# Optimization experiments

Measured on AMD Instinct MI355X. Metric: run time of the kernel, lower is better.

The kernel has to match this reference:

```python
import jax, jax.numpy as jnp
import numpy as np

SCORE_THR = 0.5
IOU_THR = 0.5
N_ANCHORS = 8400  # standard YOLO 640x640 anchor count


def setup_inputs() -> dict:
    key = jax.random.key(0)
    # [1, 5, N]: channels are (cx, cy, w, h, person_conf); uniform keeps boxes/scores in [0,1)
    yolo_raw_out = jax.random.uniform(key, (1, 5, N_ANCHORS), dtype=jnp.float32)
    return {"yolo_raw_out": yolo_raw_out}


def _pairwise_iou(b):
    # b: [N,4] xyxy
    area = (b[:, 2] - b[:, 0]) * (b[:, 3] - b[:, 1])          # [N]
    lt = jnp.maximum(b[:, None, :2], b[None, :, :2])          # [N,N,2]
    rb = jnp.minimum(b[:, None, 2:], b[None, :, 2:])          # [N,N,2]
    wh = jnp.clip(rb - lt, 0.0)
    inter = wh[..., 0] * wh[..., 1]                           # [N,N]
    union = area[:, None] + area[None, :] - inter
    return inter / jnp.maximum(union, 1e-9)


def reference(yolo_raw_out):
    # permute(0,2,1).squeeze(0) -> [N,5]
    raw = yolo_raw_out[0].T
    cx, cy, w, h = raw[:, 0], raw[:, 1], raw[:, 2], raw[:, 3]
    scores = raw[:, 4]
    # cxcywh -> xyxy (torchvision.ops.box_convert)
    xyxy = jnp.stack([cx - w / 2, cy - h / 2, cx + w / 2, cy + h / 2], axis=-1)

    valid = scores >= SCORE_THR
    # sort by score descending; invalid boxes pushed to the end
    order = jnp.argsort(-jnp.where(valid, scores, -jnp.inf))
    sb = xyxy[order]          # [N,4] sorted boxes
    ss = scores[order]        # [N]
    sv = valid[order]         # [N] score-threshold mask

    iou = _pairwise_iou(sb)   # [N,N]
    n = ss.shape[0]
    idx = jnp.arange(n)

    # Greedy NMS: in score order, an active (kept, valid) box suppresses all
    # lower-scored boxes with IoU > threshold. Faithful to torchvision.ops.nms.
    def step(keep, i):
        active = keep[i]
        suppress = (iou[i] > IOU_THR) & (idx > i) & active
        return keep & ~suppress, None

    keep, _ = jax.lax.scan(step, sv, idx)

    # Fixed-shape output: kept rows carry (x1,y1,x2,y2,score); suppressed/filtered rows zeroed.
    out = jnp.concatenate([sb, ss[:, None]], axis=1) * keep[:, None].astype(ss.dtype)
    return out
```

## Files before the change

### kernel.cpp

```cpp
#include <hip/hip_runtime.h>
#include <cstdint>

#define N_ANCH 8400
#define CBLK 132
#define SCORE_THR 0.5f
#define NDIAG 8

typedef unsigned long long u64;
typedef unsigned int u32;

__device__ __forceinline__ u64 sort_key(float s, int idx) {
  u32 k32 = (s >= SCORE_THR) ? ~__float_as_uint(s) : 0xFFFFFFFFu;
  return ((u64)k32 << 32) | (u32)idx;
}

__device__ __forceinline__ u64 rfl64(u64 v) {
  u32 lo = (u32)__builtin_amdgcn_readfirstlane((int)(u32)v);
  u32 hi = (u32)__builtin_amdgcn_readfirstlane((int)(u32)(v >> 32));
  return ((u64)hi << 32) | lo;
}

__global__ void __launch_bounds__(256) rank_kernel(const float* __restrict__ raw,
                                                   float4* __restrict__ sbox,
                                                   float* __restrict__ sscore) {
  #pragma clang fp contract(off)
  int tid = blockIdx.x * 256 + threadIdx.x;
  int wid = tid >> 6, lane = tid & 63;
  int base = wid * 4;
  float sl = raw[4 * N_ANCH + base + (lane & 3)];
  float s0 = __shfl(sl, 0), s1 = __shfl(sl, 1);
  float s2 = __shfl(sl, 2), s3 = __shfl(sl, 3);
  u64 k0 = sort_key(s0, base),     k1 = sort_key(s1, base + 1);
  u64 k2 = sort_key(s2, base + 2), k3 = sort_key(s3, base + 3);
  int c0 = 0, c1 = 0, c2 = 0, c3 = 0;
  #pragma unroll 2
  for (int j = lane; j < N_ANCH; j += 64) {
    float sj = raw[4 * N_ANCH + j];
    u64 kj = sort_key(sj, j);
    c0 += kj < k0; c1 += kj < k1; c2 += kj < k2; c3 += kj < k3;
  }
  #pragma unroll
  for (int d = 1; d < 64; d <<= 1) {
    c0 += __shfl_xor(c0, d, 64); c1 += __shfl_xor(c1, d, 64);
    c2 += __shfl_xor(c2, d, 64); c3 += __shfl_xor(c3, d, 64);
  }
  if (lane < 4) {
    int row = base + lane;
    int cnt = (lane == 0) ? c0 : (lane == 1) ? c1 : (lane == 2) ? c2 : c3;
    float sc = (lane == 0) ? s0 : (lane == 1) ? s1 : (lane == 2) ? s2 : s3;
    float cx = raw[row], cy = raw[N_ANCH + row];
    float w = raw[2 * N_ANCH + row], h = raw[3 * N_ANCH + row];
    float hw = w * 0.5f, hh = h * 0.5f;
    sbox[cnt] = make_float4(cx - hw, cy - hh, cx + hw, cy + hh);
    sscore[cnt] = sc;
  }
}

__global__ void __launch_bounds__(256) mask_kernel(const float4* __restrict__ sbox,
                                                   const float* __restrict__ sscore,
                                                   u64* __restrict__ mask,
                                                   u64* __restrict__ wlo_t) {
  #pragma clang fp contract(off)
  int cb = blockIdx.x;
  int i0 = blockIdx.y * 256;
  if (cb + 7 < (i0 >> 6)) return;
  if (!(sscore[i0] >= SCORE_THR)) return;
  if (!(sscore[cb * 64] >= SCORE_THR)) return;
  int t = threadIdx.x;
  __shared__ float4 cbox[64];
  __shared__ float carea[64];
  int j0 = cb * 64;
  if (t < 64) {
    int j = j0 + t;
    float4 bj = (j < N_ANCH) ? sbox[j] : make_float4(0.f, 0.f, 0.f, 0.f);
    cbox[t] = bj;
    carea[t] = (bj.z - bj.x) * (bj.w - bj.y);
  }
  __syncthreads();
  int i = i0 + t;
  if (i >= N_ANCH) return;
  float4 bi = sbox[i];
  float ai = (bi.z - bi.x) * (bi.w - bi.y);
  u64 wHi = 0, wLo = 0;
  for (int jj = 0; jj < 64; ++jj) {
    int jg = j0 + jj;
    float4 bb = cbox[jj];
    float ltx = fmaxf(bi.x, bb.x), lty = fmaxf(bi.y, bb.y);
    float rbx = fminf(bi.z, bb.z), rby = fminf(bi.w, bb.w);
    float wx = fmaxf(rbx - ltx, 0.f), wy = fmaxf(rby - lty, 0.f);
    float inter = wx * wy;
    float uni = (ai + carea[jj]) - inter;
    float iou = inter / fmaxf(uni, 1e-9f);
    bool sup = (iou > 0.5f) && (jg < N_ANCH);
    wHi |= (u64)(sup && (jg > i)) << jj;
    wLo |= (u64)(sup && (jg < i)) << jj;
  }
  int rb = i >> 6;
  int d = rb - cb;
  if (d < 0) {
    mask[(u64)i * CBLK + cb] = wHi;
  } else if (d < NDIAG) {
    wlo_t[((u64)d * CBLK + rb) * 64 + (i & 63)] = wLo;
  }
}

__global__ void __launch_bounds__(512, 1) nms_kernel(const float4* __restrict__ sbox,
                                                     const float* __restrict__ sscore,
                                                     const u64* __restrict__ mask,
                                                     const u64* __restrict__ wlo_t,
                                                     float* __restrict__ out) {
  __shared__ u64 keepw[CBLK + 4];
  __shared__ u64 rem[CBLK + 4];
  int tid = threadIdx.x;
  int wave = tid >> 6, lane = tid & 63;

  float s0 = sscore[lane * 132];
  u64 pb = __ballot(s0 >= SCORE_THR);
  int cnt1 = (int)__popcll(pb);
  int n_valid = 0;
  if (cnt1 > 0) {
    int a = (cnt1 - 1) * 132 + 1;
    int i1 = a + 3 * lane;
    float t1 = (i1 + 0 < N_ANCH) ? sscore[i1 + 0] : -1.f;
    float t2 = (i1 + 1 < N_ANCH) ? sscore[i1 + 1] : -1.f;
    float t3 = (i1 + 2 < N_ANCH) ? sscore[i1 + 2] : -1.f;
    u64 q1 = __ballot(t1 >= SCORE_THR);
    u64 q2 = __ballot(t2 >= SCORE_THR);
    u64 q3 = __ballot(t3 >= SCORE_THR);
    n_valid = a + (int)__popcll(q1) + (int)__popcll(q2) + (int)__popcll(q3);
  }
  int VB = (n_valid + 63) >> 6;
  int NG = (VB + 3) >> 2;

  for (int b = tid; b < CBLK + 4; b += 512) { keepw[b] = 0; rem[b] = 0; }

  int rs = (wave - 1) * 37;
  int nr = 256 - rs; if (nr > 37) nr = 37;

  u64 cur[26], nxt[26];
  auto wt = [&](int d, int b) -> u64 {
    return wlo_t[((u64)d * CBLK + b) * 64 + lane];
  };
  auto load_w0 = [&](int g, u64* R) {
    int b = 4 * g;
    bool k1 = (b + 1 < VB), k2 = (b + 2 < VB), k3 = (b + 3 < VB);
    R[0] = wt(0, b);
    R[1] = k1 ? wt(0, b + 1) : 0ull;
    R[2] = k2 ? wt(0, b + 2) : 0ull;
    R[3] = k3 ? wt(0, b + 3) : 0ull;
    R[4] = k1 ? wt(1, b + 1) : 0ull;
    R[5] = k2 ? wt(2, b + 2) : 0ull;
    R[6] = k2 ? wt(1, b + 2) : 0ull;
    R[7] = k3 ? wt(3, b + 3) : 0ull;
    R[8] = k3 ? wt(2, b + 3) : 0ull;
    R[9] = k3 ? wt(1, b + 3) : 0ull;
    #pragma unroll
    for (int m = 0; m < 4; ++m) {
      int c = b + 4 + m;
      bool ok = (c < VB);
      #pragma unroll
      for (int j = 0; j < 4; ++j)
        R[10 + m * 4 + j] = ok ? wt(4 + m - j, c) : 0ull;
    }
  };
  auto fixpoint = [&](u64 colw, u64 act) -> u64 {
    u64 U = act, K = 0;
    while (U) {
      u64 covered = __ballot((colw & U) != 0ull);
      u64 nk = U & ~covered;
      u64 supp = __ballot((colw & nk) != 0ull);
      K |= nk;
      U &= ~(nk | supp);
    }
    return K;
  };

  u64 P0 = 0, P1 = 0, P2 = 0, P3 = 0;

  if (wave == 0 && NG > 0) load_w0(0, cur);

  for (int g = 0; g < NG; ++g) {
    asm volatile("s_waitcnt lgkmcnt(0)\ns_barrier" ::: "memory");

    if (wave == 0) {
      __builtin_amdgcn_s_setprio(1);
      int b = 4 * g;
      u64 r0 = rem[b], r1 = rem[b + 1], r2 = rem[b + 2], r3 = rem[b + 3];
      if (g > 0) {
        #pragma unroll
        for (int i = 0; i < 26; ++i) cur[i] = nxt[i];
      }
      if (g + 1 < NG) load_w0(g + 1, nxt);

      int remn = n_valid - b * 64;
      u64 vm0, vm1, vm2, vm3;
      {
        int m0 = remn, m1 = remn - 64, m2 = remn - 128, m3 = remn - 192;
        vm0 = (m0 >= 64) ? ~0ull : ((m0 <= 0) ? 0ull : ((1ull << m0) - 1ull));
        vm1 = (m1 >= 64) ? ~0ull : ((m1 <= 0) ? 0ull : ((1ull << m1) - 1ull));
        vm2 = (m2 >= 64) ? ~0ull : ((m2 <= 0) ? 0ull : ((1ull << m2) - 1ull));
        vm3 = (m3 >= 64) ? ~0ull : ((m3 <= 0) ? 0ull : ((1ull << m3) - 1ull));
      }
      u64 act0 = vm0 & ~(rfl64(r0) | P0);
      u64 act1 = vm1 & ~(rfl64(r1) | P1);
      u64 act2 = vm2 & ~(rfl64(r2) | P2);
      u64 act3 = vm3 & ~(rfl64(r3) | P3);

      u64 kw0 = fixpoint(cur[0], act0);
      u64 s1 = __ballot((cur[4] & kw0) != 0ull);
      u64 kw1 = fixpoint(cur[1], act1 & ~s1);
      u64 s2 = __ballot(((cur[5] & kw0) | (cur[6] & kw1)) != 0ull);
      u64 kw2 = fixpoint(cur[2], act2 & ~s2);
      u64 s3 = __ballot(((cur[7] & kw0) | (cur[8] & kw1) | (cur[9] & kw2)) != 0ull);
      u64 kw3 = fixpoint(cur[3], act3 & ~s3);

      if (lane == 0) {
        keepw[b] = kw0; keepw[b + 1] = kw1;
        keepw[b + 2] = kw2; keepw[b + 3] = kw3;
      }

      P0 = __ballot(((cur[10] & kw0) | (cur[11] & kw1) |
                     (cur[12] & kw2) | (cur[13] & kw3)) != 0ull);
      P1 = __ballot(((cur[14] & kw0) | (cur[15] & kw1) |
                     (cur[16] & kw2) | (cur[17] & kw3)) != 0ull);
      P2 = __ballot(((cur[18] & kw0) | (cur[19] & kw1) |
                     (cur[20] & kw2) | (cur[21] & kw3)) != 0ull);
      P3 = __ballot(((cur[22] & kw0) | (cur[23] & kw1) |
                     (cur[24] & kw2) | (cur[25] & kw3)) != 0ull);
      __builtin_amdgcn_s_setprio(0);
    } else if (g >= 1) {
      int e = g - 1;
      int base = 4 * e + 8;
      if (base < VB) {
        int wi = rs >> 6, sh = rs & 63;
        u64 lo = keepw[4 * e + wi];
        u64 hi = (sh + nr > 64 && wi < 3) ? keepw[4 * e + wi + 1] : 0ull;
        u64 window = sh ? ((lo >> sh) | (hi << (64 - sh))) : lo;
        window = rfl64(window);
        const u64* pr = mask + (u64)(256 * e + rs) * CBLK;
        int cL = base + lane;
        bool okL = (cL < VB);
        u64 acc = 0;
        #pragma unroll
        for (int r = 0; r < 37; ++r) {
          bool bit = (r < nr) && (((window >> r) & 1ull) != 0ull);
          u64 v = (bit && okL) ? pr[(u64)r * CBLK + cL] : 0ull;
          acc |= v;
        }
        if (okL && acc) atomicOr((unsigned long long*)&rem[cL], acc);
        if (base + 64 < VB) {
          int cH = cL + 64;
          bool okH = (cH < VB);
          u64 acc2 = 0;
          #pragma unroll
          for (int r = 0; r < 37; ++r) {
            bool bit = (r < nr) && (((window >> r) & 1ull) != 0ull);
            u64 v = (bit && okH) ? pr[(u64)r * CBLK + cH] : 0ull;
            acc2 |= v;
          }
          if (okH && acc2) atomicOr((unsigned long long*)&rem[cH], acc2);
        }
      }
    }
  }
  __syncthreads();

  for (int r2 = tid; r2 < N_ANCH; r2 += 512) {
    u64 kv = keepw[r2 >> 6];
    bool kp = (kv >> (r2 & 63)) & 1ull;
    float4 b4 = sbox[r2];
    float sc = sscore[r2];
    float* o = out + r2 * 5;
    o[0] = kp ? b4.x : 0.f;
    o[1] = kp ? b4.y : 0.f;
    o[2] = kp ? b4.z : 0.f;
    o[3] = kp ? b4.w : 0.f;
    o[4] = kp ? sc : 0.f;
  }
}

extern "C" void kernel_launch(void* const* d_in, const int* in_sizes, int n_in,
                              void* d_out, int out_size, void* d_ws, size_t ws_size,
                              hipStream_t stream) {
  const float* raw = (const float*)d_in[0];
  float* out = (float*)d_out;
  char* ws = (char*)d_ws;
  float4* sbox = (float4*)ws;
  float* sscore = (float*)(ws + 8448 * 16);
  u64* mask = (u64*)(ws + 8448 * 16 + 8448 * 4);
  u64* wlo_t = (u64*)(ws + 8448 * 16 + 8448 * 4 + (size_t)N_ANCH * CBLK * 8);

  rank_kernel<<<525, 256, 0, stream>>>(raw, sbox, sscore);
  mask_kernel<<<dim3(CBLK, 33), 256, 0, stream>>>(sbox, sscore, mask, wlo_t);
  nms_kernel<<<1, 512, 0, stream>>>(sbox, sscore, mask, wlo_t, out);
}
```

Before: 131.6 us.

## Merge four per-word NMS fixpoints into one joint loop; vectorize rank score loads

The serial NMS resolver in wave 0 used to run four fixpoint loops one after another, each block word waiting on the previous one. It now iterates all four words together, so the ballots for different words can overlap and the serial chain of dependent iterations gets shorter. Each round may do more ballots, since it always evaluates all four words. Separately, the rank kernel reads scores as float4 and compares four candidates per lane per iteration, cutting load instructions and loop trips.

```diff
diff --git a/kernel.cpp b/kernel.cpp
--- a/kernel.cpp
+++ b/kernel.cpp
@@ -27,17 +27,22 @@
   int tid = blockIdx.x * 256 + threadIdx.x;
   int wid = tid >> 6, lane = tid & 63;
   int base = wid * 4;
-  float sl = raw[4 * N_ANCH + base + (lane & 3)];
-  float s0 = __shfl(sl, 0), s1 = __shfl(sl, 1);
-  float s2 = __shfl(sl, 2), s3 = __shfl(sl, 3);
-  u64 k0 = sort_key(s0, base),     k1 = sort_key(s1, base + 1);
-  u64 k2 = sort_key(s2, base + 2), k3 = sort_key(s3, base + 3);
+  const float* sc = raw + 4 * N_ANCH;
+  float4 sv = *(const float4*)(sc + base);
+  u64 k0 = sort_key(sv.x, base),     k1 = sort_key(sv.y, base + 1);
+  u64 k2 = sort_key(sv.z, base + 2), k3 = sort_key(sv.w, base + 3);
   int c0 = 0, c1 = 0, c2 = 0, c3 = 0;
-  #pragma unroll 2
-  for (int j = lane; j < N_ANCH; j += 64) {
-    float sj = raw[4 * N_ANCH + j];
-    u64 kj = sort_key(sj, j);
-    c0 += kj < k0; c1 += kj < k1; c2 += kj < k2; c3 += kj < k3;
+  for (int it = 0; it < 33; ++it) {
+    int j = it * 256 + (lane << 2);
+    if (j < N_ANCH) {
+      float4 q = *(const float4*)(sc + j);
+      u64 a0 = sort_key(q.x, j),     a1 = sort_key(q.y, j + 1);
+      u64 a2 = sort_key(q.z, j + 2), a3 = sort_key(q.w, j + 3);
+      c0 += (a0 < k0) + (a1 < k0) + (a2 < k0) + (a3 < k0);
+      c1 += (a0 < k1) + (a1 < k1) + (a2 < k1) + (a3 < k1);
+      c2 += (a0 < k2) + (a1 < k2) + (a2 < k2) + (a3 < k2);
+      c3 += (a0 < k3) + (a1 < k3) + (a2 < k3) + (a3 < k3);
+    }
   }
   #pragma unroll
   for (int d = 1; d < 64; d <<= 1) {
@@ -47,12 +52,12 @@
   if (lane < 4) {
     int row = base + lane;
     int cnt = (lane == 0) ? c0 : (lane == 1) ? c1 : (lane == 2) ? c2 : c3;
-    float sc = (lane == 0) ? s0 : (lane == 1) ? s1 : (lane == 2) ? s2 : s3;
+    float s = (lane == 0) ? sv.x : (lane == 1) ? sv.y : (lane == 2) ? sv.z : sv.w;
     float cx = raw[row], cy = raw[N_ANCH + row];
     float w = raw[2 * N_ANCH + row], h = raw[3 * N_ANCH + row];
     float hw = w * 0.5f, hh = h * 0.5f;
     sbox[cnt] = make_float4(cx - hw, cy - hh, cx + hw, cy + hh);
-    sscore[cnt] = sc;
+    sscore[cnt] = s;
   }
 }
 
@@ -163,17 +168,6 @@
         R[10 + m * 4 + j] = ok ? wt(4 + m - j, c) : 0ull;
     }
   };
-  auto fixpoint = [&](u64 colw, u64 act) -> u64 {
-    u64 U = act, K = 0;
-    while (U) {
-      u64 covered = __ballot((colw & U) != 0ull);
-      u64 nk = U & ~covered;
-      u64 supp = __ballot((colw & nk) != 0ull);
-      K |= nk;
-      U &= ~(nk | supp);
-    }
-    return K;
-  };
 
   u64 P0 = 0, P1 = 0, P2 = 0, P3 = 0;
 
@@ -201,18 +195,32 @@
         vm2 = (m2 >= 64) ? ~0ull : ((m2 <= 0) ? 0ull : ((1ull << m2) - 1ull));
         vm3 = (m3 >= 64) ? ~0ull : ((m3 <= 0) ? 0ull : ((1ull << m3) - 1ull));
       }
-      u64 act0 = vm0 & ~(rfl64(r0) | P0);
-      u64 act1 = vm1 & ~(rfl64(r1) | P1);
-      u64 act2 = vm2 & ~(rfl64(r2) | P2);
-      u64 act3 = vm3 & ~(rfl64(r3) | P3);
-
-      u64 kw0 = fixpoint(cur[0], act0);
-      u64 s1 = __ballot((cur[4] & kw0) != 0ull);
-      u64 kw1 = fixpoint(cur[1], act1 & ~s1);
-      u64 s2 = __ballot(((cur[5] & kw0) | (cur[6] & kw1)) != 0ull);
-      u64 kw2 = fixpoint(cur[2], act2 & ~s2);
-      u64 s3 = __ballot(((cur[7] & kw0) | (cur[8] & kw1) | (cur[9] & kw2)) != 0ull);
-      u64 kw3 = fixpoint(cur[3], act3 & ~s3);
+      u64 U0 = vm0 & ~(rfl64(r0) | P0);
+      u64 U1 = vm1 & ~(rfl64(r1) | P1);
+      u64 U2 = vm2 & ~(rfl64(r2) | P2);
+      u64 U3 = vm3 & ~(rfl64(r3) | P3);
+
+      u64 K0 = 0, K1 = 0, K2 = 0, K3 = 0;
+      while (U0 | U1 | U2 | U3) {
+        u64 p0 = cur[0] & U0;
+        u64 p1 = (cur[4] & U0) | (cur[1] & U1);
+        u64 p2 = (cur[5] & U0) | (cur[6] & U1) | (cur[2] & U2);
+        u64 p3 = (cur[7] & U0) | (cur[8] & U1) | (cur[9] & U2) | (cur[3] & U3);
+        u64 c0 = __ballot(p0 != 0ull);
+        u64 c1 = __ballot(p1 != 0ull);
+        u64 c2 = __ballot(p2 != 0ull);
+        u64 c3 = __ballot(p3 != 0ull);
+        u64 n0 = U0 & ~c0, n1 = U1 & ~c1, n2 = U2 & ~c2, n3 = U3 & ~c3;
+        u64 s0 = __ballot((cur[0] & n0) != 0ull);
+        u64 s1 = __ballot(((cur[4] & n0) | (cur[1] & n1)) != 0ull);
+        u64 s2 = __ballot(((cur[5] & n0) | (cur[6] & n1) | (cur[2] & n2)) != 0ull);
+        u64 s3 = __ballot(((cur[7] & n0) | (cur[8] & n1) | (cur[9] & n2) |
+                           (cur[3] & n3)) != 0ull);
+        K0 |= n0; K1 |= n1; K2 |= n2; K3 |= n3;
+        U0 &= ~(n0 | s0); U1 &= ~(n1 | s1);
+        U2 &= ~(n2 | s2); U3 &= ~(n3 | s3);
+      }
+      u64 kw0 = K0, kw1 = K1, kw2 = K2, kw3 = K3;
 
       if (lane == 0) {
         keepw[b] = kw0; keepw[b + 1] = kw1;
```

Result: no change. 133.8 us (+1.7%).

## Fuse rank, mask and NMS stages into one cooperative kernel with grid syncs

Applied to the files above, without the earlier changes.

Merges the three launches into a single cooperative kernel of 256 blocks that runs the ranking, mask building and serial NMS phases, separated by grid-wide syncs, with the NMS done by block 0. This removes two kernel launch gaps and the inter-kernel drain. The ranking loop also switches to float4 loads that compare four candidates per lane. In exchange, grid.sync carries its own cost, mask tiles are now 512 rows per task with a strided task loop, and the old three-kernel path is kept as a fallback if the cooperative launch fails.

```diff
diff --git a/kernel.cpp b/kernel.cpp
--- a/kernel.cpp
+++ b/kernel.cpp
@@ -1,10 +1,14 @@
 #include <hip/hip_runtime.h>
+#include <hip/hip_cooperative_groups.h>
 #include <cstdint>
 
 #define N_ANCH 8400
 #define CBLK 132
 #define SCORE_THR 0.5f
 #define NDIAG 8
+#define NBLK 256
+
+namespace cg = cooperative_groups;
 
 typedef unsigned long long u64;
 typedef unsigned int u32;
@@ -20,24 +24,29 @@
   return ((u64)hi << 32) | lo;
 }
 
-__global__ void __launch_bounds__(256) rank_kernel(const float* __restrict__ raw,
-                                                   float4* __restrict__ sbox,
-                                                   float* __restrict__ sscore) {
+
+__device__ __forceinline__ void rank_task(const float* __restrict__ raw,
+                                          float4* __restrict__ sbox,
+                                          float* __restrict__ sscore,
+                                          int t5, int lane) {
   #pragma clang fp contract(off)
-  int tid = blockIdx.x * 256 + threadIdx.x;
-  int wid = tid >> 6, lane = tid & 63;
-  int base = wid * 4;
-  float sl = raw[4 * N_ANCH + base + (lane & 3)];
-  float s0 = __shfl(sl, 0), s1 = __shfl(sl, 1);
-  float s2 = __shfl(sl, 2), s3 = __shfl(sl, 3);
-  u64 k0 = sort_key(s0, base),     k1 = sort_key(s1, base + 1);
-  u64 k2 = sort_key(s2, base + 2), k3 = sort_key(s3, base + 3);
+  const float* sc = raw + 4 * N_ANCH;
+  int base = t5 * 4;
+  float4 sv = *(const float4*)(sc + base);
+  u64 k0 = sort_key(sv.x, base),     k1 = sort_key(sv.y, base + 1);
+  u64 k2 = sort_key(sv.z, base + 2), k3 = sort_key(sv.w, base + 3);
   int c0 = 0, c1 = 0, c2 = 0, c3 = 0;
-  #pragma unroll 2
-  for (int j = lane; j < N_ANCH; j += 64) {
-    float sj = raw[4 * N_ANCH + j];
-    u64 kj = sort_key(sj, j);
-    c0 += kj < k0; c1 += kj < k1; c2 += kj < k2; c3 += kj < k3;
+  for (int it = 0; it < 33; ++it) {
+    int j = it * 256 + (lane << 2);
+    if (j < N_ANCH) {
+      float4 q = *(const float4*)(sc + j);
+      u64 a0 = sort_key(q.x, j),     a1 = sort_key(q.y, j + 1);
+      u64 a2 = sort_key(q.z, j + 2), a3 = sort_key(q.w, j + 3);
+      c0 += (a0 < k0) + (a1 < k0) + (a2 < k0) + (a3 < k0);
+      c1 += (a0 < k1) + (a1 < k1) + (a2 < k1) + (a3 < k1);
+      c2 += (a0 < k2) + (a1 < k2) + (a2 < k2) + (a3 < k2);
+      c3 += (a0 < k3) + (a1 < k3) + (a2 < k3) + (a3 < k3);
+    }
   }
   #pragma unroll
   for (int d = 1; d < 64; d <<= 1) {
@@ -47,38 +56,22 @@
   if (lane < 4) {
     int row = base + lane;
     int cnt = (lane == 0) ? c0 : (lane == 1) ? c1 : (lane == 2) ? c2 : c3;
-    float sc = (lane == 0) ? s0 : (lane == 1) ? s1 : (lane == 2) ? s2 : s3;
+    float s = (lane == 0) ? sv.x : (lane == 1) ? sv.y : (lane == 2) ? sv.z : sv.w;
     float cx = raw[row], cy = raw[N_ANCH + row];
     float w = raw[2 * N_ANCH + row], h = raw[3 * N_ANCH + row];
     float hw = w * 0.5f, hh = h * 0.5f;
     sbox[cnt] = make_float4(cx - hw, cy - hh, cx + hw, cy + hh);
-    sscore[cnt] = sc;
-  }
-}
-
-__global__ void __launch_bounds__(256) mask_kernel(const float4* __restrict__ sbox,
-                                                   const float* __restrict__ sscore,
-                                                   u64* __restrict__ mask,
-                                                   u64* __restrict__ wlo_t) {
+    sscore[cnt] = s;
+  }
+}
+
+__device__ __forceinline__ void mask_row(const float4* __restrict__ sbox,
+                                         u64* __restrict__ mask,
+                                         u64* __restrict__ wlo_t,
+                                         const float4* cbox, const float* carea,
+                                         int i, int cb) {
   #pragma clang fp contract(off)
-  int cb = blockIdx.x;
-  int i0 = blockIdx.y * 256;
-  if (cb + 7 < (i0 >> 6)) return;
-  if (!(sscore[i0] >= SCORE_THR)) return;
-  if (!(sscore[cb * 64] >= SCORE_THR)) return;
-  int t = threadIdx.x;
-  __shared__ float4 cbox[64];
-  __shared__ float carea[64];
   int j0 = cb * 64;
-  if (t < 64) {
-    int j = j0 + t;
-    float4 bj = (j < N_ANCH) ? sbox[j] : make_float4(0.f, 0.f, 0.f, 0.f);
-    cbox[t] = bj;
-    carea[t] = (bj.z - bj.x) * (bj.w - bj.y);
-  }
-  __syncthreads();
-  int i = i0 + t;
-  if (i >= N_ANCH) return;
   float4 bi = sbox[i];
   float ai = (bi.z - bi.x) * (bi.w - bi.y);
   u64 wHi = 0, wLo = 0;
@@ -104,16 +97,13 @@
   }
 }
 
-__global__ void __launch_bounds__(512, 1) nms_kernel(const float4* __restrict__ sbox,
-                                                     const float* __restrict__ sscore,
-                                                     const u64* __restrict__ mask,
-                                                     const u64* __restrict__ wlo_t,
-                                                     float* __restrict__ out) {
-  __shared__ u64 keepw[CBLK + 4];
-  __shared__ u64 rem[CBLK + 4];
-  int tid = threadIdx.x;
-  int wave = tid >> 6, lane = tid & 63;
-
+__device__ void nms_body(const float4* __restrict__ sbox,
+                         const float* __restrict__ sscore,
+                         const u64* __restrict__ mask,
+                         const u64* __restrict__ wlo_t,
+                         float* __restrict__ out,
+                         u64* keepw, u64* rem,
+                         int tid, int wave, int lane) {
   float s0 = sscore[lane * 132];
   u64 pb = __ballot(s0 >= SCORE_THR);
   int cnt1 = (int)__popcll(pb);
@@ -279,6 +269,98 @@
   }
 }
 
+__global__ void __launch_bounds__(512, 1) fused_kernel(
+    const float* __restrict__ raw,
+    float4* __restrict__ sbox, float* __restrict__ sscore,
+    u64* __restrict__ mask, u64* __restrict__ wlo_t,
+    float* __restrict__ out) {
+  cg::grid_group grid = cg::this_grid();
+  int bid = blockIdx.x;
+  int tid = threadIdx.x;
+  int wave = tid >> 6, lane = tid & 63;
+
+  __shared__ float4 cbox[64];
+  __shared__ float carea[64];
+  __shared__ u64 keepw[CBLK + 4];
+  __shared__ u64 rem[CBLK + 4];
+
+  for (int t5 = bid * 8 + wave; t5 < 2100; t5 += 2048)
+    rank_task(raw, sbox, sscore, t5, lane);
+
+  __threadfence();
+  grid.sync();
+
+  for (int task = bid; task < CBLK * 17; task += NBLK) {
+    int sb = task / CBLK;
+    int cb = task - sb * CBLK;
+    int i0 = sb * 512;
+    bool active = !(cb + 7 < (i0 >> 6)) &&
+                  (sscore[i0] >= SCORE_THR) &&
+                  (sscore[cb * 64] >= SCORE_THR);
+    __syncthreads();
+    if (active && tid < 64) {
+      int j = cb * 64 + tid;
+      float4 bj = (j < N_ANCH) ? sbox[j] : make_float4(0.f, 0.f, 0.f, 0.f);
+      cbox[tid] = bj;
+      carea[tid] = (bj.z - bj.x) * (bj.w - bj.y);
+    }
+    __syncthreads();
+    if (active) {
+      int i = i0 + tid;
+      if (i < N_ANCH) mask_row(sbox, mask, wlo_t, cbox, carea, i, cb);
+    }
+  }
+
+  __threadfence();
+  grid.sync();
+
+  if (bid != 0) return;
+  nms_body(sbox, sscore, mask, wlo_t, out, keepw, rem, tid, wave, lane);
+}
+
+__global__ void __launch_bounds__(256) rank_kernel(const float* __restrict__ raw,
+                                                   float4* __restrict__ sbox,
+                                                   float* __restrict__ sscore) {
+  int tid = blockIdx.x * 256 + threadIdx.x;
+  int wid = tid >> 6, lane = tid & 63;
+  if (wid < 2100) rank_task(raw, sbox, sscore, wid, lane);
+}
+
+__global__ void __launch_bounds__(256) mask_kernel(const float4* __restrict__ sbox,
+                                                   const float* __restrict__ sscore,
+                                                   u64* __restrict__ mask,
+                                                   u64* __restrict__ wlo_t) {
+  int cb = blockIdx.x;
+  int i0 = blockIdx.y * 256;
+  if (cb + 7 < (i0 >> 6)) return;
+  if (!(sscore[i0] >= SCORE_THR)) return;
+  if (!(sscore[cb * 64] >= SCORE_THR)) return;
+  int t = threadIdx.x;
+  __shared__ float4 cbox[64];
+  __shared__ float carea[64];
+  if (t < 64) {
+    int j = cb * 64 + t;
+    float4 bj = (j < N_ANCH) ? sbox[j] : make_float4(0.f, 0.f, 0.f, 0.f);
+    cbox[t] = bj;
+    carea[t] = (bj.z - bj.x) * (bj.w - bj.y);
+  }
+  __syncthreads();
+  int i = i0 + t;
+  if (i >= N_ANCH) return;
+  mask_row(sbox, mask, wlo_t, cbox, carea, i, cb);
+}
+
+__global__ void __launch_bounds__(512, 1) nms_kernel(const float4* __restrict__ sbox,
+                                                     const float* __restrict__ sscore,
+                                                     const u64* __restrict__ mask,
+                                                     const u64* __restrict__ wlo_t,
+                                                     float* __restrict__ out) {
+  __shared__ u64 keepw[CBLK + 4];
+  __shared__ u64 rem[CBLK + 4];
+  int tid = threadIdx.x;
+  nms_body(sbox, sscore, mask, wlo_t, out, keepw, rem, tid, tid >> 6, tid & 63);
+}
+
 extern "C" void kernel_launch(void* const* d_in, const int* in_sizes, int n_in,
                               void* d_out, int out_size, void* d_ws, size_t ws_size,
                               hipStream_t stream) {
@@ -290,7 +372,14 @@
   u64* mask = (u64*)(ws + 8448 * 16 + 8448 * 4);
   u64* wlo_t = (u64*)(ws + 8448 * 16 + 8448 * 4 + (size_t)N_ANCH * CBLK * 8);
 
-  rank_kernel<<<525, 256, 0, stream>>>(raw, sbox, sscore);
-  mask_kernel<<<dim3(CBLK, 33), 256, 0, stream>>>(sbox, sscore, mask, wlo_t);
-  nms_kernel<<<1, 512, 0, stream>>>(sbox, sscore, mask, wlo_t, out);
-}
+  void* args[] = {(void*)&raw, (void*)&sbox, (void*)&sscore,
+                  (void*)&mask, (void*)&wlo_t, (void*)&out};
+  hipError_t err = hipLaunchCooperativeKernel((const void*)fused_kernel,
+                                              dim3(NBLK), dim3(512),
+                                              args, 0, stream);
+  if (err != hipSuccess) {
+    rank_kernel<<<525, 256, 0, stream>>>(raw, sbox, sscore);
+    mask_kernel<<<dim3(CBLK, 33), 256, 0, stream>>>(sbox, sscore, mask, wlo_t);
+    nms_kernel<<<1, 512, 0, stream>>>(sbox, sscore, mask, wlo_t, out);
+  }
+}
```

Result: slower. 255.8 us (+94.4%).

## Vectorize rank score loads and widen NMS kernel to 1024 threads

Applied to the files above, without the earlier changes.

The rank kernel now reads scores as float4, both for the four row keys and in the counting loop, so each lane compares four keys per iteration and issues fewer loads. The single-block NMS kernel grows from 512 to 1024 threads. The mask-reduction rows are split across 15 helper waves of 18 rows each instead of 7 waves of 37, which shortens each wave's serial chain of dependent loads. The wider block may raise register pressure on the 26-entry register arrays, and any wave whose row range falls past 256 now skips the reduction.

```diff
diff --git a/kernel.cpp b/kernel.cpp
--- a/kernel.cpp
+++ b/kernel.cpp
@@ -27,17 +27,22 @@
   int tid = blockIdx.x * 256 + threadIdx.x;
   int wid = tid >> 6, lane = tid & 63;
   int base = wid * 4;
-  float sl = raw[4 * N_ANCH + base + (lane & 3)];
-  float s0 = __shfl(sl, 0), s1 = __shfl(sl, 1);
-  float s2 = __shfl(sl, 2), s3 = __shfl(sl, 3);
-  u64 k0 = sort_key(s0, base),     k1 = sort_key(s1, base + 1);
-  u64 k2 = sort_key(s2, base + 2), k3 = sort_key(s3, base + 3);
+  const float* sc = raw + 4 * N_ANCH;
+  float4 sv = *(const float4*)(sc + base);
+  u64 k0 = sort_key(sv.x, base),     k1 = sort_key(sv.y, base + 1);
+  u64 k2 = sort_key(sv.z, base + 2), k3 = sort_key(sv.w, base + 3);
   int c0 = 0, c1 = 0, c2 = 0, c3 = 0;
-  #pragma unroll 2
-  for (int j = lane; j < N_ANCH; j += 64) {
-    float sj = raw[4 * N_ANCH + j];
-    u64 kj = sort_key(sj, j);
-    c0 += kj < k0; c1 += kj < k1; c2 += kj < k2; c3 += kj < k3;
+  for (int it = 0; it < 33; ++it) {
+    int j = it * 256 + (lane << 2);
+    if (j < N_ANCH) {
+      float4 q = *(const float4*)(sc + j);
+      u64 a0 = sort_key(q.x, j),     a1 = sort_key(q.y, j + 1);
+      u64 a2 = sort_key(q.z, j + 2), a3 = sort_key(q.w, j + 3);
+      c0 += (a0 < k0) + (a1 < k0) + (a2 < k0) + (a3 < k0);
+      c1 += (a0 < k1) + (a1 < k1) + (a2 < k1) + (a3 < k1);
+      c2 += (a0 < k2) + (a1 < k2) + (a2 < k2) + (a3 < k2);
+      c3 += (a0 < k3) + (a1 < k3) + (a2 < k3) + (a3 < k3);
+    }
   }
   #pragma unroll
   for (int d = 1; d < 64; d <<= 1) {
@@ -47,12 +52,12 @@
   if (lane < 4) {
     int row = base + lane;
     int cnt = (lane == 0) ? c0 : (lane == 1) ? c1 : (lane == 2) ? c2 : c3;
-    float sc = (lane == 0) ? s0 : (lane == 1) ? s1 : (lane == 2) ? s2 : s3;
+    float s = (lane == 0) ? sv.x : (lane == 1) ? sv.y : (lane == 2) ? sv.z : sv.w;
     float cx = raw[row], cy = raw[N_ANCH + row];
     float w = raw[2 * N_ANCH + row], h = raw[3 * N_ANCH + row];
     float hw = w * 0.5f, hh = h * 0.5f;
     sbox[cnt] = make_float4(cx - hw, cy - hh, cx + hw, cy + hh);
-    sscore[cnt] = sc;
+    sscore[cnt] = s;
   }
 }
 
@@ -104,11 +109,11 @@
   }
 }
 
-__global__ void __launch_bounds__(512, 1) nms_kernel(const float4* __restrict__ sbox,
-                                                     const float* __restrict__ sscore,
-                                                     const u64* __restrict__ mask,
-                                                     const u64* __restrict__ wlo_t,
-                                                     float* __restrict__ out) {
+__global__ void __launch_bounds__(1024, 1) nms_kernel(const float4* __restrict__ sbox,
+                                                      const float* __restrict__ sscore,
+                                                      const u64* __restrict__ mask,
+                                                      const u64* __restrict__ wlo_t,
+                                                      float* __restrict__ out) {
   __shared__ u64 keepw[CBLK + 4];
   __shared__ u64 rem[CBLK + 4];
   int tid = threadIdx.x;
@@ -132,10 +137,10 @@
   int VB = (n_valid + 63) >> 6;
   int NG = (VB + 3) >> 2;
 
-  for (int b = tid; b < CBLK + 4; b += 512) { keepw[b] = 0; rem[b] = 0; }
-
-  int rs = (wave - 1) * 37;
-  int nr = 256 - rs; if (nr > 37) nr = 37;
+  for (int b = tid; b < CBLK + 4; b += 1024) { keepw[b] = 0; rem[b] = 0; }
+
+  int rs = (wave - 1) * 18;
+  int nr = 256 - rs; if (nr > 18) nr = 18; if (nr < 0) nr = 0;
 
   u64 cur[26], nxt[26];
   auto wt = [&](int d, int b) -> u64 {
@@ -228,7 +233,7 @@
       P3 = __ballot(((cur[22] & kw0) | (cur[23] & kw1) |
                      (cur[24] & kw2) | (cur[25] & kw3)) != 0ull);
       __builtin_amdgcn_s_setprio(0);
-    } else if (g >= 1) {
+    } else if (g >= 1 && nr > 0) {
       int e = g - 1;
       int base = 4 * e + 8;
       if (base < VB) {
@@ -242,7 +247,7 @@
         bool okL = (cL < VB);
         u64 acc = 0;
         #pragma unroll
-        for (int r = 0; r < 37; ++r) {
+        for (int r = 0; r < 18; ++r) {
           bool bit = (r < nr) && (((window >> r) & 1ull) != 0ull);
           u64 v = (bit && okL) ? pr[(u64)r * CBLK + cL] : 0ull;
           acc |= v;
@@ -253,7 +258,7 @@
           bool okH = (cH < VB);
           u64 acc2 = 0;
           #pragma unroll
-          for (int r = 0; r < 37; ++r) {
+          for (int r = 0; r < 18; ++r) {
             bool bit = (r < nr) && (((window >> r) & 1ull) != 0ull);
             u64 v = (bit && okH) ? pr[(u64)r * CBLK + cH] : 0ull;
             acc2 |= v;
@@ -265,7 +270,7 @@
   }
   __syncthreads();
 
-  for (int r2 = tid; r2 < N_ANCH; r2 += 512) {
+  for (int r2 = tid; r2 < N_ANCH; r2 += 1024) {
     u64 kv = keepw[r2 >> 6];
     bool kp = (kv >> (r2 & 63)) & 1ull;
     float4 b4 = sbox[r2];
@@ -292,5 +297,5 @@
 
   rank_kernel<<<525, 256, 0, stream>>>(raw, sbox, sscore);
   mask_kernel<<<dim3(CBLK, 33), 256, 0, stream>>>(sbox, sscore, mask, wlo_t);
-  nms_kernel<<<1, 512, 0, stream>>>(sbox, sscore, mask, wlo_t, out);
-}
+  nms_kernel<<<1, 1024, 0, stream>>>(sbox, sscore, mask, wlo_t, out);
+}
```

Result: slower. 169.1 us (+28.5%).
